# Performance work log

Hardware: AMD Instinct MI355X
Metric: run time of the kernel (lower is better)

Reference implementation:

```python
import jax, jax.numpy as jnp
import numpy as np

B, L, D, H = 2, 2048, 1024, 16
DH = D // H
EPS = 1e-5


def setup_inputs() -> dict:
    key = jax.random.key(0)
    ks = jax.random.split(key, 8)
    s = 0.02  # realistic init scale for weights
    # causal mask: True where attention is DISALLOWED (masked_fill semantics)
    mask = jnp.triu(jnp.ones((L, L), dtype=bool), k=1)[None, None]  # [1,1,L,L]
    return {
        "x": jax.random.normal(ks[0], (B, L, D), jnp.float32),
        "mask": mask,
        "ln_g": jnp.ones((D,), jnp.float32),
        "ln_b": jnp.zeros((D,), jnp.float32),
        "Wq": jax.random.normal(ks[1], (D, D), jnp.float32) * s,
        "bq": jnp.zeros((D,), jnp.float32),
        "Wk": jax.random.normal(ks[2], (D, D), jnp.float32) * s,
        "bk": jnp.zeros((D,), jnp.float32),
        "Wv": jax.random.normal(ks[3], (D, D), jnp.float32) * s,
        "bv": jnp.zeros((D,), jnp.float32),
        "Wo": jax.random.normal(ks[4], (D, D), jnp.float32) * s,
        "bo": jnp.zeros((D,), jnp.float32),
    }


def _layernorm(x, g, b):
    mu = jnp.mean(x, axis=-1, keepdims=True)
    var = jnp.var(x, axis=-1, keepdims=True)
    return (x - mu) * jax.lax.rsqrt(var + EPS) * g + b


def reference(x, mask, ln_g, ln_b, Wq, bq, Wk, bk, Wv, bv, Wo, bo):
    b, l, d = x.shape
    h = _layernorm(x, ln_g, ln_b)
    # separate Q/K/V linears, split into heads: [b, H, l, DH]
    q = (h @ Wq + bq).reshape(b, l, H, DH).transpose(0, 2, 1, 3)
    k = (h @ Wk + bk).reshape(b, l, H, DH).transpose(0, 2, 1, 3)
    v = (h @ Wv + bv).reshape(b, l, H, DH).transpose(0, 2, 1, 3)
    scale = jnp.asarray(DH, x.dtype) ** -0.5
    # full L x L score matrix (this is exactly what the torch module does)
    w = jnp.einsum("bhqd,bhkd->bhqk", q, k) * scale
    w = jnp.where(mask, -jnp.inf, w)
    w = jax.nn.softmax(w, axis=-1)
    # dropout layers are identity in eval mode
    o = jnp.einsum("bhqk,bhkd->bhqd", w, v)
    o = o.transpose(0, 2, 1, 3).reshape(b, l, d)
    return o @ Wo + bo
```

## Files before the change

### kernel.cpp

```cpp
#include <hip/hip_runtime.h>
#include <hip/hip_bf16.h>


typedef __bf16  bf16x8 __attribute__((ext_vector_type(8)));
typedef __bf16  bf16x4 __attribute__((ext_vector_type(4)));
typedef float   f32x4  __attribute__((ext_vector_type(4)));
typedef float   f32x16 __attribute__((ext_vector_type(16)));
typedef unsigned int u32x2 __attribute__((ext_vector_type(2)));
typedef unsigned int u32x4 __attribute__((ext_vector_type(4)));

#define MFMA16(a, b, c) __builtin_amdgcn_mfma_f32_16x16x32_bf16(a, b, c, 0, 0, 0)
#define MFMA32(a, b, c) __builtin_amdgcn_mfma_f32_32x32x16_bf16(a, b, c, 0, 0, 0)

#define LDT 72
#define LDO 68

#define QSCALE 0.18033688011112042f

__device__ __forceinline__ void gl_lds16(const void* g, void* l) {
    __builtin_amdgcn_global_load_lds(
        (const __attribute__((address_space(1))) void*)g,
        (__attribute__((address_space(3))) void*)l, 16, 0, 0);
}

__global__ __launch_bounds__(256) void prep_kernel(
    const float* __restrict__ x, const float* __restrict__ g,
    const float* __restrict__ bta, __hip_bfloat16* __restrict__ h,
    const float* __restrict__ Wq, const float* __restrict__ Wk,
    const float* __restrict__ Wv, const float* __restrict__ Wo,
    __hip_bfloat16* __restrict__ tq, __hip_bfloat16* __restrict__ tk,
    __hip_bfloat16* __restrict__ tv, __hip_bfloat16* __restrict__ to_)
{
    __shared__ float red[8];
    __shared__ float tbuf[32][33];

    if (blockIdx.z == 0) {
        const int row = blockIdx.x, t = threadIdx.x;
        const float* xr = x + (size_t)row * 1024;
        const float4 xv = *(const float4*)(xr + t * 4);
        float s  = xv.x + xv.y + xv.z + xv.w;
        float ss = xv.x * xv.x + xv.y * xv.y + xv.z * xv.z + xv.w * xv.w;
        #pragma unroll
        for (int off = 32; off > 0; off >>= 1) {
            s  += __shfl_down(s, off);
            ss += __shfl_down(ss, off);
        }
        const int lane = t & 63, wave = t >> 6;
        if (lane == 0) { red[wave] = s; red[4 + wave] = ss; }
        __syncthreads();
        const float S  = red[0] + red[1] + red[2] + red[3];
        const float SS = red[4] + red[5] + red[6] + red[7];
        const float mu   = S * (1.0f / 1024.0f);
        const float var  = SS * (1.0f / 1024.0f) - mu * mu;
        const float rstd = rsqrtf(var + 1e-5f);
        const float4 gv = *(const float4*)(g + t * 4);
        const float4 bv = *(const float4*)(bta + t * 4);
        bf16x4 hv;
        hv[0] = (__bf16)((xv.x - mu) * rstd * gv.x + bv.x);
        hv[1] = (__bf16)((xv.y - mu) * rstd * gv.y + bv.y);
        hv[2] = (__bf16)((xv.z - mu) * rstd * gv.z + bv.z);
        hv[3] = (__bf16)((xv.w - mu) * rstd * gv.w + bv.w);
        *(bf16x4*)(h + (size_t)row * 1024 + t * 4) = hv;
    } else {
        const int idx = blockIdx.x;
        const int z  = idx >> 10;
        const int tt = idx & 1023;
        const int n0 = (tt & 31) * 32, k0 = (tt >> 5) * 32;
        const float* src = (z == 0) ? Wq : (z == 1) ? Wk : (z == 2) ? Wv : Wo;
        __hip_bfloat16* dst = (z == 0) ? tq : (z == 1) ? tk : (z == 2) ? tv : to_;
        const int tr = threadIdx.x >> 5;
        const int tc = threadIdx.x & 31;
        #pragma unroll
        for (int p = 0; p < 4; ++p)
            tbuf[p * 8 + tr][tc] = src[(size_t)(k0 + p * 8 + tr) * 1024 + n0 + tc];
        __syncthreads();
        #pragma unroll
        for (int p = 0; p < 4; ++p)
            dst[(size_t)(n0 + p * 8 + tr) * 1024 + k0 + tc] =
                __float2bfloat16(tbuf[tc][p * 8 + tr]);
    }
}

__device__ __forceinline__ void gemm_core_1024(
    const __hip_bfloat16* __restrict__ A, const __hip_bfloat16* __restrict__ Bt,
    int m0, int n0, f32x4 (&acc)[4][2])
{
    __shared__ __align__(16) __hip_bfloat16 sA[128 * 64];
    __shared__ __align__(16) __hip_bfloat16 sB[128 * 64];
    const int tid  = threadIdx.x;
    const int wave = tid >> 6, lane = tid & 63;
    const int quad = lane >> 4, l16 = lane & 15;
    const int wm = wave >> 2, wn = wave & 3;

    const f32x4 zero = {0.f, 0.f, 0.f, 0.f};
    #pragma unroll
    for (int i = 0; i < 4; ++i)
        #pragma unroll
        for (int j = 0; j < 2; ++j) acc[i][j] = zero;

    const int r0 = tid >> 3;
    const int c0 = (((tid & 7) ^ (r0 & 7)) << 3);
    const __hip_bfloat16* Ap = A  + (size_t)(m0 + r0) * 1024 + c0;
    const __hip_bfloat16* Bp = Bt + (size_t)(n0 + r0) * 1024 + c0;
    __hip_bfloat16* lA0 = sA + tid * 8;
    __hip_bfloat16* lB0 = sB + tid * 8;

    const int rsw = l16 & 7;

    for (int k0 = 0; k0 < 1024; k0 += 64) {
        __syncthreads();
        gl_lds16(Ap + k0, lA0);
        gl_lds16(Ap + (size_t)64 * 1024 + k0, lA0 + 64 * 64);
        gl_lds16(Bp + k0, lB0);
        gl_lds16(Bp + (size_t)64 * 1024 + k0, lB0 + 64 * 64);
        __syncthreads();
        #pragma unroll
        for (int kk = 0; kk < 64; kk += 32) {
            const int sl = (((quad + (kk >> 3)) ^ rsw) << 3);
            bf16x8 af[4], bfr[2];
            #pragma unroll
            for (int mt = 0; mt < 4; ++mt)
                af[mt] = *(const bf16x8*)(sA + (wm * 64 + mt * 16 + l16) * 64 + sl);
            #pragma unroll
            for (int nt = 0; nt < 2; ++nt)
                bfr[nt] = *(const bf16x8*)(sB + (wn * 32 + nt * 16 + l16) * 64 + sl);
            #pragma unroll
            for (int mt = 0; mt < 4; ++mt)
                #pragma unroll
                for (int nt = 0; nt < 2; ++nt)
                    acc[mt][nt] = MFMA16(af[mt], bfr[nt], acc[mt][nt]);
        }
    }
}

__global__ __launch_bounds__(512) void gemm_qkv_kernel(
    const __hip_bfloat16* __restrict__ h,
    const __hip_bfloat16* __restrict__ wt_base,
    const float* __restrict__ bq, const float* __restrict__ bk,
    const float* __restrict__ bv,
    __hip_bfloat16* __restrict__ qkv_base)
{
    const int z = blockIdx.z;
    const __hip_bfloat16* wt = wt_base + ((size_t)z << 20);
    __hip_bfloat16* outp = qkv_base + ((size_t)z << 22);

    const bool swp = (z == 2);
    const __hip_bfloat16* A  = swp ? wt : h;
    const __hip_bfloat16* Bt = swp ? h  : wt;
    const int m0 = swp ? blockIdx.x * 128 : blockIdx.y * 128;
    const int n0 = swp ? blockIdx.y * 128 : blockIdx.x * 128;

    f32x4 acc[4][2];
    gemm_core_1024(A, Bt, m0, n0, acc);

    const int lane = threadIdx.x & 63, wave = threadIdx.x >> 6;
    const int quad = lane >> 4, l16 = lane & 15;
    const int wm = wave >> 2, wn = wave & 3;

    if (!swp) {
        const float* bias = (z == 0) ? bq : bk;
        const float scale = (z == 0) ? QSCALE : 1.0f;
        #pragma unroll
        for (int mt = 0; mt < 4; ++mt)
            #pragma unroll
            for (int nt = 0; nt < 2; ++nt)
                #pragma unroll
                for (int r = 0; r < 4; ++r) {
                    const int gm = m0 + wm * 64 + mt * 16 + quad * 4 + r;
                    const int gn = n0 + wn * 32 + nt * 16 + l16;
                    const float v = (acc[mt][nt][r] + bias[gn]) * scale;
                    const int b = gm >> 11, l = gm & 2047;
                    const int hh = gn >> 6, dh = gn & 63;
                    outp[(((((size_t)(b * 16 + hh)) << 11) + l) * 64) + dh] = __float2bfloat16(v);
                }
    } else {
        #pragma unroll
        for (int mt = 0; mt < 4; ++mt)
            #pragma unroll
            for (int nt = 0; nt < 2; ++nt)
                #pragma unroll
                for (int r = 0; r < 4; ++r) {
                    const int rr = m0 + wm * 64 + mt * 16 + quad * 4 + r;
                    const int cc = n0 + wn * 32 + nt * 16 + l16;
                    const float v = acc[mt][nt][r] + bv[rr];
                    const int b = cc >> 11, l = cc & 2047;
                    const int hh = rr >> 6, dh = rr & 63;
                    outp[((((size_t)(b * 16 + hh)) * 64 + dh) << 11) + l] = __float2bfloat16(v);
                }
    }
}

__global__ __launch_bounds__(512) void gemm_out_kernel(
    const __hip_bfloat16* __restrict__ o, const __hip_bfloat16* __restrict__ wot,
    const float* __restrict__ bo, float* __restrict__ out)
{
    __shared__ __align__(16) __hip_bfloat16 sA[64 * 64];
    __shared__ __align__(16) __hip_bfloat16 sB[128 * 64];
    const int tid  = threadIdx.x;
    const int wave = tid >> 6, lane = tid & 63;
    const int quad = lane >> 4, l16 = lane & 15;
    const int wm = wave >> 2, wn = wave & 3;
    const int m0 = blockIdx.y * 64, n0 = blockIdx.x * 128;

    const f32x4 zero = {0.f, 0.f, 0.f, 0.f};
    f32x4 acc[2][2];
    #pragma unroll
    for (int i = 0; i < 2; ++i)
        #pragma unroll
        for (int j = 0; j < 2; ++j) acc[i][j] = zero;

    const int r0 = tid >> 3;
    const int c0 = (((tid & 7) ^ (r0 & 7)) << 3);
    const __hip_bfloat16* Ap = o   + (size_t)(m0 + r0) * 1024 + c0;
    const __hip_bfloat16* Bp = wot + (size_t)(n0 + r0) * 1024 + c0;
    __hip_bfloat16* lA0 = sA + tid * 8;
    __hip_bfloat16* lB0 = sB + tid * 8;

    const int rsw = l16 & 7;

    for (int k0 = 0; k0 < 1024; k0 += 64) {
        __syncthreads();
        gl_lds16(Ap + k0, lA0);
        gl_lds16(Bp + k0, lB0);
        gl_lds16(Bp + (size_t)64 * 1024 + k0, lB0 + 64 * 64);
        __syncthreads();
        #pragma unroll
        for (int kk = 0; kk < 64; kk += 32) {
            const int sl = (((quad + (kk >> 3)) ^ rsw) << 3);
            bf16x8 af[2], bfr[2];
            #pragma unroll
            for (int mt = 0; mt < 2; ++mt)
                af[mt] = *(const bf16x8*)(sA + (wm * 32 + mt * 16 + l16) * 64 + sl);
            #pragma unroll
            for (int nt = 0; nt < 2; ++nt)
                bfr[nt] = *(const bf16x8*)(sB + (wn * 32 + nt * 16 + l16) * 64 + sl);
            #pragma unroll
            for (int mt = 0; mt < 2; ++mt)
                #pragma unroll
                for (int nt = 0; nt < 2; ++nt)
                    acc[mt][nt] = MFMA16(af[mt], bfr[nt], acc[mt][nt]);
        }
    }

    #pragma unroll
    for (int mt = 0; mt < 2; ++mt)
        #pragma unroll
        for (int nt = 0; nt < 2; ++nt)
            #pragma unroll
            for (int r = 0; r < 4; ++r) {
                const int gm = m0 + wm * 32 + mt * 16 + quad * 4 + r;
                const int gn = n0 + wn * 32 + nt * 16 + l16;
                out[(size_t)gm * 1024 + gn] = acc[mt][nt][r] + bo[gn];
            }
}

__global__ __launch_bounds__(256, 4) void attn_kernel(
    const __hip_bfloat16* __restrict__ Q,
    const __hip_bfloat16* __restrict__ Kg,
    const __hip_bfloat16* __restrict__ Vt,
    __hip_bfloat16* __restrict__ O)
{
    __shared__ __align__(16) char smem[36864];
    __hip_bfloat16* sK = (__hip_bfloat16*)smem;
    __hip_bfloat16* sV = (__hip_bfloat16*)(smem + 18432);

    const int tid  = threadIdx.x;
    const int wave = tid >> 6, lane = tid & 63;
    const int wk = wave >> 1, wq = wave & 1;
    const int q5 = lane & 31, hi = lane >> 5;
    const int bh = blockIdx.x;
    const int qt = 31 - blockIdx.y;
    const int q0 = qt * 64;

    const __hip_bfloat16* Qp = Q  + (size_t)bh * 2048 * 64;
    const __hip_bfloat16* Kp = Kg + (size_t)bh * 2048 * 64;
    const __hip_bfloat16* Vp = Vt + (size_t)bh * 64 * 2048;

    bf16x8 Qf[4];
    #pragma unroll
    for (int ks = 0; ks < 4; ++ks)
        Qf[ks] = *(const bf16x8*)(Qp + (size_t)(q0 + wq * 32 + q5) * 64 + ks * 16 + hi * 8);

    f32x16 o0, o1;
    #pragma unroll
    for (int r = 0; r < 16; ++r) { o0[r] = 0.f; o1[r] = 0.f; }
    float l_run = 0.f;

    const int qloc = wq * 32 + q5;

    auto stage = [&](int j, int buf) {
        const int k0 = j * 64;
        __hip_bfloat16* dK = sK + buf * (64 * LDT);
        __hip_bfloat16* dV = sV + buf * (64 * LDT);
        #pragma unroll
        for (int i = 0; i < 2; ++i) {
            const int chunk = tid + 256 * i, rr = chunk >> 3, cc = (chunk & 7) << 3;
            *(int4*)(dK + rr * LDT + cc) = *(const int4*)(Kp + (size_t)(k0 + rr) * 64 + cc);
            *(int4*)(dV + rr * LDT + cc) = *(const int4*)(Vp + (size_t)rr * 2048 + k0 + cc);
        }
    };

    stage(0, 0);

    for (int j = 0; j <= qt; ++j) {
        const int cur = j & 1;
        __syncthreads();
        if (j < qt) stage(j + 1, cur ^ 1);

        const __hip_bfloat16* sKg = sK + cur * (64 * LDT);
        const __hip_bfloat16* sVg = sV + cur * (64 * LDT);
        const bool diag = (j == qt);
        f32x16 s;
        #pragma unroll
        for (int i = 0; i < 16; ++i) s[i] = 0.f;
        __builtin_amdgcn_s_setprio(1);
        #pragma unroll
        for (int ks = 0; ks < 4; ++ks) {
            const bf16x8 kf = *(const bf16x8*)(sKg + (wk * 32 + q5) * LDT + ks * 16 + hi * 8);
            s = MFMA32(kf, Qf[ks], s);
        }
        __builtin_amdgcn_s_setprio(0);
        if (diag) {
            #pragma unroll
            for (int i = 0; i < 16; ++i) {
                const int krow = wk * 32 + (i & 3) + 8 * (i >> 2) + 4 * hi;
                if (krow > qloc) s[i] = -1e30f;
            }
        }
        float rs = 0.f;
        u32x2 U[4];
        #pragma unroll
        for (int rb = 0; rb < 4; ++rb) {
            bf16x4 pk;
            #pragma unroll
            for (int c = 0; c < 4; ++c) {
                const float p = exp2f(s[rb * 4 + c]);
                rs += p;
                pk[c] = (__bf16)p;
            }
            U[rb] = __builtin_bit_cast(u32x2, pk);
        }
        rs += __shfl_xor(rs, 32);
        l_run += rs;
        __builtin_amdgcn_s_setprio(1);
        #pragma unroll
        for (int t = 0; t < 2; ++t) {
            const unsigned p0a = __shfl_xor(U[2 * t][0], 32);
            const unsigned p0b = __shfl_xor(U[2 * t][1], 32);
            const unsigned p1a = __shfl_xor(U[2 * t + 1][0], 32);
            const unsigned p1b = __shfl_xor(U[2 * t + 1][1], 32);
            const unsigned w0 = hi ? p1a : U[2 * t][0];
            const unsigned w1 = hi ? p1b : U[2 * t][1];
            const unsigned w2 = hi ? U[2 * t + 1][0] : p0a;
            const unsigned w3 = hi ? U[2 * t + 1][1] : p0b;
            const u32x4 pw = {w0, w1, w2, w3};
            const bf16x8 pf = __builtin_bit_cast(bf16x8, pw);
            const bf16x8 vf0 = *(const bf16x8*)(sVg + (q5)      * LDT + wk * 32 + 16 * t + 8 * hi);
            const bf16x8 vf1 = *(const bf16x8*)(sVg + (32 + q5) * LDT + wk * 32 + 16 * t + 8 * hi);
            o0 = MFMA32(vf0, pf, o0);
            o1 = MFMA32(vf1, pf, o1);
        }
        __builtin_amdgcn_s_setprio(0);
    }

    __syncthreads();
    float* Oscr = (float*)smem;
    float* lscr = (float*)(smem + 17408);

    if (hi == 0)
        lscr[wk * 64 + wq * 32 + q5] = l_run;

    auto wrO = [&](bool add) {
        float* rowp = Oscr + (wq * 32 + q5) * LDO;
        #pragma unroll
        for (int d = 0; d < 2; ++d) {
            const f32x16& oc = d ? o1 : o0;
            #pragma unroll
            for (int rb = 0; rb < 4; ++rb) {
                float* p = rowp + d * 32 + 8 * rb + 4 * hi;
                f32x4 v;
                if (add) {
                    v = *(const f32x4*)p;
                    v[0] += oc[rb * 4 + 0]; v[1] += oc[rb * 4 + 1];
                    v[2] += oc[rb * 4 + 2]; v[3] += oc[rb * 4 + 3];
                } else {
                    v[0] = oc[rb * 4 + 0]; v[1] = oc[rb * 4 + 1];
                    v[2] = oc[rb * 4 + 2]; v[3] = oc[rb * 4 + 3];
                }
                *(f32x4*)p = v;
            }
        }
    };
    if (wk == 1) wrO(false);
    __syncthreads();
    if (wk == 0) wrO(true);
    __syncthreads();

    const int b = bh >> 4, hh = bh & 15;
    #pragma unroll
    for (int i = 0; i < 2; ++i) {
        const int chunk = tid + 256 * i;
        const int row = chunk >> 3, col = (chunk & 7) << 3;
        const float lt = lscr[0 * 64 + row] + lscr[1 * 64 + row];
        const float linv = 1.0f / lt;
        const float* src = Oscr + row * LDO + col;
        const f32x4 v0 = *(const f32x4*)src;
        const f32x4 v1 = *(const f32x4*)(src + 4);
        bf16x8 ov;
        ov[0] = (__bf16)(v0[0] * linv); ov[1] = (__bf16)(v0[1] * linv);
        ov[2] = (__bf16)(v0[2] * linv); ov[3] = (__bf16)(v0[3] * linv);
        ov[4] = (__bf16)(v1[0] * linv); ov[5] = (__bf16)(v1[1] * linv);
        ov[6] = (__bf16)(v1[2] * linv); ov[7] = (__bf16)(v1[3] * linv);
        *(bf16x8*)(O + ((size_t)b * 2048 + q0 + row) * 1024 + hh * 64 + col) = ov;
    }
}

extern "C" void kernel_launch(void* const* d_in, const int* in_sizes, int n_in,
                              void* d_out, int out_size, void* d_ws, size_t ws_size,
                              hipStream_t stream) {
    const float* x    = (const float*)d_in[0];
    const float* ln_g = (const float*)d_in[2];
    const float* ln_b = (const float*)d_in[3];
    const float* Wq = (const float*)d_in[4];  const float* bq = (const float*)d_in[5];
    const float* Wk = (const float*)d_in[6];  const float* bk = (const float*)d_in[7];
    const float* Wv = (const float*)d_in[8];  const float* bv = (const float*)d_in[9];
    const float* Wo = (const float*)d_in[10]; const float* bo = (const float*)d_in[11];
    float* out = (float*)d_out;

    __hip_bfloat16* ws = (__hip_bfloat16*)d_ws;
    const size_t M1 = 1024 * 1024;
    __hip_bfloat16* h   = ws;
    __hip_bfloat16* wqt = ws + 4 * M1;
    __hip_bfloat16* wot = ws + 7 * M1;
    __hip_bfloat16* q   = ws + 8 * M1;
    __hip_bfloat16* k   = ws + 12 * M1;
    __hip_bfloat16* vt  = ws + 16 * M1;
    __hip_bfloat16* o   = h;

    prep_kernel<<<dim3(4096, 1, 2), 256, 0, stream>>>(
        x, ln_g, ln_b, h, Wq, Wk, Wv, Wo, wqt, wqt + M1, wqt + 2 * M1, wot);
    gemm_qkv_kernel<<<dim3(8, 32, 3), 512, 0, stream>>>(h, wqt, bq, bk, bv, q);
    attn_kernel<<<dim3(32, 32), 256, 0, stream>>>(q, k, vt, o);
    gemm_out_kernel<<<dim3(8, 64), 512, 0, stream>>>(o, wot, bo, out);
}
```

Baseline: 194.3 us.

## Split long causal query tiles across two blocks with atomic-counter merge

The 16 longest causal query tiles per head are each split into two KV halves processed by separate blocks, enlarging the grid from 32x32 to 32x48. Each half writes normalized output and its row sums; an atomic counter lets the last-finishing block merge the partner's result. The goal is to reduce load imbalance and tail latency from triangular causal work. The cost is an extra bf16 round-trip of partial outputs (precision loss), threadfences, and a counter reset added to the prep kernel.

```diff
diff --git a/kernel.cpp b/kernel.cpp
--- a/kernel.cpp
+++ b/kernel.cpp
@@ -29,7 +29,8 @@
     const float* __restrict__ Wq, const float* __restrict__ Wk,
     const float* __restrict__ Wv, const float* __restrict__ Wo,
     __hip_bfloat16* __restrict__ tq, __hip_bfloat16* __restrict__ tk,
-    __hip_bfloat16* __restrict__ tv, __hip_bfloat16* __restrict__ to_)
+    __hip_bfloat16* __restrict__ tv, __hip_bfloat16* __restrict__ to_,
+    int* __restrict__ cnt)
 {
     __shared__ float red[8];
     __shared__ float tbuf[32][33];
@@ -63,6 +64,10 @@
         *(bf16x4*)(h + (size_t)row * 1024 + t * 4) = hv;
     } else {
         const int idx = blockIdx.x;
+        if (idx == 0) {
+            cnt[threadIdx.x] = 0;
+            cnt[threadIdx.x + 256] = 0;
+        }
         const int z  = idx >> 10;
         const int tt = idx & 1023;
         const int n0 = (tt & 31) * 32, k0 = (tt >> 5) * 32;
@@ -258,9 +263,13 @@
     const __hip_bfloat16* __restrict__ Q,
     const __hip_bfloat16* __restrict__ Kg,
     const __hip_bfloat16* __restrict__ Vt,
-    __hip_bfloat16* __restrict__ O)
+    __hip_bfloat16* __restrict__ O,
+    __hip_bfloat16* __restrict__ Opart,
+    float* __restrict__ lpart,
+    int* __restrict__ cnt)
 {
     __shared__ __align__(16) char smem[36864];
+    __shared__ int svar;
     __hip_bfloat16* sK = (__hip_bfloat16*)smem;
     __hip_bfloat16* sV = (__hip_bfloat16*)(smem + 18432);
 
@@ -268,9 +277,15 @@
     const int wave = tid >> 6, lane = tid & 63;
     const int wk = wave >> 1, wq = wave & 1;
     const int q5 = lane & 31, hi = lane >> 5;
-    const int bh = blockIdx.x;
-    const int qt = 31 - blockIdx.y;
-    const int q0 = qt * 64;
+    const int bh = blockIdx.x, y = blockIdx.y;
+
+    const bool split = (y < 32);
+    const int qt   = split ? (31 - (y >> 1)) : (47 - y);
+    const int half = split ? (y & 1) : 0;
+    const int hsp  = (qt + 1) >> 1;
+    const int j0   = (split && half) ? hsp : 0;
+    const int j1   = (split && !half) ? (hsp - 1) : qt;
+    const int q0   = qt * 64;
 
     const __hip_bfloat16* Qp = Q  + (size_t)bh * 2048 * 64;
     const __hip_bfloat16* Kp = Kg + (size_t)bh * 2048 * 64;
@@ -300,12 +315,12 @@
         }
     };
 
-    stage(0, 0);
-
-    for (int j = 0; j <= qt; ++j) {
-        const int cur = j & 1;
-        __syncthreads();
-        if (j < qt) stage(j + 1, cur ^ 1);
+    stage(j0, 0);
+
+    for (int j = j0; j <= j1; ++j) {
+        const int cur = (j - j0) & 1;
+        __syncthreads();
+        if (j < j1) stage(j + 1, cur ^ 1);
 
         const __hip_bfloat16* sKg = sK + cur * (64 * LDT);
         const __hip_bfloat16* sVg = sV + cur * (64 * LDT);
@@ -397,21 +412,78 @@
     __syncthreads();
 
     const int b = bh >> 4, hh = bh & 15;
-    #pragma unroll
-    for (int i = 0; i < 2; ++i) {
-        const int chunk = tid + 256 * i;
-        const int row = chunk >> 3, col = (chunk & 7) << 3;
-        const float lt = lscr[0 * 64 + row] + lscr[1 * 64 + row];
-        const float linv = 1.0f / lt;
-        const float* src = Oscr + row * LDO + col;
-        const f32x4 v0 = *(const f32x4*)src;
-        const f32x4 v1 = *(const f32x4*)(src + 4);
-        bf16x8 ov;
-        ov[0] = (__bf16)(v0[0] * linv); ov[1] = (__bf16)(v0[1] * linv);
-        ov[2] = (__bf16)(v0[2] * linv); ov[3] = (__bf16)(v0[3] * linv);
-        ov[4] = (__bf16)(v1[0] * linv); ov[5] = (__bf16)(v1[1] * linv);
-        ov[6] = (__bf16)(v1[2] * linv); ov[7] = (__bf16)(v1[3] * linv);
-        *(bf16x8*)(O + ((size_t)b * 2048 + q0 + row) * 1024 + hh * 64 + col) = ov;
+
+    if (!split) {
+        #pragma unroll
+        for (int i = 0; i < 2; ++i) {
+            const int chunk = tid + 256 * i;
+            const int row = chunk >> 3, col = (chunk & 7) << 3;
+            const float lt = lscr[row] + lscr[64 + row];
+            const float linv = 1.0f / lt;
+            const float* src = Oscr + row * LDO + col;
+            const f32x4 v0 = *(const f32x4*)src;
+            const f32x4 v1 = *(const f32x4*)(src + 4);
+            bf16x8 ov;
+            ov[0] = (__bf16)(v0[0] * linv); ov[1] = (__bf16)(v0[1] * linv);
+            ov[2] = (__bf16)(v0[2] * linv); ov[3] = (__bf16)(v0[3] * linv);
+            ov[4] = (__bf16)(v1[0] * linv); ov[5] = (__bf16)(v1[1] * linv);
+            ov[6] = (__bf16)(v1[2] * linv); ov[7] = (__bf16)(v1[3] * linv);
+            *(bf16x8*)(O + ((size_t)b * 2048 + q0 + row) * 1024 + hh * 64 + col) = ov;
+        }
+    } else {
+        const int tidx = bh * 16 + (qt - 16);
+        #pragma unroll
+        for (int i = 0; i < 2; ++i) {
+            const int chunk = tid + 256 * i;
+            const int row = chunk >> 3, col = (chunk & 7) << 3;
+            const float lo = lscr[row] + lscr[64 + row];
+            const float linv = 1.0f / lo;
+            const float* src = Oscr + row * LDO + col;
+            const f32x4 v0 = *(const f32x4*)src;
+            const f32x4 v1 = *(const f32x4*)(src + 4);
+            bf16x8 ov;
+            ov[0] = (__bf16)(v0[0] * linv); ov[1] = (__bf16)(v0[1] * linv);
+            ov[2] = (__bf16)(v0[2] * linv); ov[3] = (__bf16)(v0[3] * linv);
+            ov[4] = (__bf16)(v1[0] * linv); ov[5] = (__bf16)(v1[1] * linv);
+            ov[6] = (__bf16)(v1[2] * linv); ov[7] = (__bf16)(v1[3] * linv);
+            if (half == 0)
+                *(bf16x8*)(O + ((size_t)b * 2048 + q0 + row) * 1024 + hh * 64 + col) = ov;
+            else
+                *(bf16x8*)(Opart + (size_t)tidx * 4096 + row * 64 + col) = ov;
+        }
+        if (tid < 64)
+            lpart[(tidx * 2 + half) * 64 + tid] = lscr[tid] + lscr[64 + tid];
+
+        __threadfence();
+        __syncthreads();
+        if (tid == 0) svar = atomicAdd(&cnt[tidx], 1);
+        __syncthreads();
+        if (svar == 1) {
+            __threadfence();
+            #pragma unroll
+            for (int i = 0; i < 2; ++i) {
+                const int chunk = tid + 256 * i;
+                const int row = chunk >> 3, col = (chunk & 7) << 3;
+                const float lo = lscr[row] + lscr[64 + row];
+                const float lp = lpart[(tidx * 2 + (half ^ 1)) * 64 + row];
+                const float winv = 1.0f / (lo + lp);
+                const float* src = Oscr + row * LDO + col;
+                const f32x4 v0 = *(const f32x4*)src;
+                const f32x4 v1 = *(const f32x4*)(src + 4);
+                bf16x8 pv;
+                if (half == 0)
+                    pv = *(const bf16x8*)(Opart + (size_t)tidx * 4096 + row * 64 + col);
+                else
+                    pv = *(const bf16x8*)(O + ((size_t)b * 2048 + q0 + row) * 1024 + hh * 64 + col);
+                bf16x8 ov;
+                #pragma unroll
+                for (int e = 0; e < 8; ++e) {
+                    const float own = (e < 4) ? v0[e] : v1[e - 4];
+                    ov[e] = (__bf16)((own + (float)pv[e] * lp) * winv);
+                }
+                *(bf16x8*)(O + ((size_t)b * 2048 + q0 + row) * 1024 + hh * 64 + col) = ov;
+            }
+        }
     }
 }
 
@@ -436,10 +508,13 @@
     __hip_bfloat16* k   = ws + 12 * M1;
     __hip_bfloat16* vt  = ws + 16 * M1;
     __hip_bfloat16* o   = h;
+    __hip_bfloat16* opart = wqt;
+    float* lpart = (float*)(ws + 6 * M1);
+    int*   cnt   = (int*)(ws + 20 * M1);
 
     prep_kernel<<<dim3(4096, 1, 2), 256, 0, stream>>>(
-        x, ln_g, ln_b, h, Wq, Wk, Wv, Wo, wqt, wqt + M1, wqt + 2 * M1, wot);
+        x, ln_g, ln_b, h, Wq, Wk, Wv, Wo, wqt, wqt + M1, wqt + 2 * M1, wot, cnt);
     gemm_qkv_kernel<<<dim3(8, 32, 3), 512, 0, stream>>>(h, wqt, bq, bk, bv, q);
-    attn_kernel<<<dim3(32, 32), 256, 0, stream>>>(q, k, vt, o);
+    attn_kernel<<<dim3(32, 48), 256, 0, stream>>>(q, k, vt, o, opart, lpart, cnt);
     gemm_out_kernel<<<dim3(8, 64), 512, 0, stream>>>(o, wot, bo, out);
 }
```

Result: slower. 342.1 us (+76.0%).
